# Performance work log

Measured on AMD Instinct MI355X. Metric: run time of the kernel, lower is better.

The kernel has to match this reference:

```python
import jax, jax.numpy as jnp
import numpy as np

B, C, H, W = 4, 2048, 48, 48
HC = 256

def setup_inputs() -> dict:
    key = jax.random.key(0)
    k1, k2, k3, k4 = jax.random.split(key, 4)
    scale = 1.0 / np.sqrt(C)
    return {
        "left_features": jax.random.normal(k1, (B, C, H, W), dtype=jnp.float32),
        "right_features": jax.random.normal(k2, (B, C, H, W), dtype=jnp.float32),
        "Wq": jax.random.normal(k3, (HC, C), dtype=jnp.float32) * scale,
        "bq": jnp.zeros((HC,), dtype=jnp.float32),
        "Wk": jax.random.normal(k4, (HC, C), dtype=jnp.float32) * scale,
        "bk": jnp.zeros((HC,), dtype=jnp.float32),
    }

def _coattn(query_feat, ref_feat, Wq, bq, Wk, bk):
    b, c, h, w = query_feat.shape
    hw = h * w
    # 1x1 convs == per-pixel channel projections
    Q = jnp.einsum('bchw,oc->bohw', query_feat, Wq) + bq[None, :, None, None]
    K = jnp.einsum('bchw,oc->bohw', ref_feat, Wk) + bk[None, :, None, None]
    Qf = Q.reshape(b, -1, hw)          # [b, hc, hw_q]
    Kf = K.reshape(b, -1, hw)          # [b, hc, hw_k]
    V = ref_feat.reshape(b, c, hw)     # [b, c, hw_k]
    # attention scores over all spatial pairs, softmax over reference positions
    attn = jax.nn.softmax(jnp.einsum('bci,bcj->bij', Qf, Kf), axis=-1)  # [b, hw_q, hw_k]
    out = jnp.einsum('bij,bcj->bci', attn, V)  # [b, c, hw_q]
    return out.reshape(b, c, h, w)

def reference(left_features, right_features, Wq, bq, Wk, bk):
    weighted_r = _coattn(left_features, right_features, Wq, bq, Wk, bk)
    weighted_l = _coattn(right_features, left_features, Wq, bq, Wk, bk)
    # rearrange '[orig, weighted] two b c h w -> b (two c) h w' == channel concat
    left_attended = jnp.concatenate([left_features, weighted_l], axis=1)
    right_attended = jnp.concatenate([right_features, weighted_r], axis=1)
    return (left_attended, right_attended)
```

## Files before the change

kernel.cpp:

```cpp
#include <hip/hip_runtime.h>
#include <stdint.h>


#define NB 4
#define NC 2048
#define NHW 2304
#define NHC 256
#define NT 36

typedef _Float16 f16;
typedef __attribute__((ext_vector_type(4))) _Float16 f16x4;
typedef __attribute__((ext_vector_type(8))) _Float16 f16x8;
typedef __attribute__((ext_vector_type(4))) float f32x4;

static __device__ __forceinline__ void glds16(const void* g, void* lds) {
  __builtin_amdgcn_global_load_lds(
      (const __attribute__((address_space(1))) uint32_t*)g,
      (__attribute__((address_space(3))) uint32_t*)lds, 16, 0, 0);
}

__global__ __launch_bounds__(256) void k_prep(
    const float* __restrict__ xl, const float* __restrict__ xr,
    float* __restrict__ out, f16* __restrict__ Xh, f16* __restrict__ Xt) {
  const int z = blockIdx.z, side = z >> 2, b = z & 3;
  const float* X = (side ? xr : xl) + (size_t)b * NC * NHW;
  const int hw0 = blockIdx.x * 64, c0 = blockIdx.y * 64;
  const int t = threadIdx.x;
  const int colb = (t & 15) * 4;
  const int r0 = t >> 4;
  __shared__ f16 Lt[64 * 64];
  float* outb = out + (size_t)side * ((size_t)NB * 2 * NC * NHW) + (size_t)b * (2 * NC * NHW);
  f16* Xhb = Xh + (size_t)side * ((size_t)NB * NC * NHW) + (size_t)b * NC * NHW;
  f16* Xtb = Xt + (size_t)side * ((size_t)NB * NHW * NC) + (size_t)b * NHW * NC;
#pragma unroll
  for (int p = 0; p < 4; ++p) {
    int r = r0 + p * 16;
    size_t go = (size_t)(c0 + r) * NHW + hw0 + colb;
    float4 v = *(const float4*)&X[go];
    *(float4*)&outb[go] = v;
    f16x4 h; h[0] = (f16)v.x; h[1] = (f16)v.y; h[2] = (f16)v.z; h[3] = (f16)v.w;
    *(f16x4*)&Xhb[go] = h;
#pragma unroll
    for (int j = 0; j < 4; ++j) {
      int row = colb + j;
      int byte = row * 128 + ((r * 2) ^ ((((row >> 2) & 7)) << 4));
      *(f16*)((char*)Lt + byte) = h[j];
    }
  }
  __syncthreads();
#pragma unroll
  for (int p = 0; p < 2; ++p) {
    int idx = p * 256 + t;
    int row = idx >> 3, ch = idx & 7;
    int byte = row * 128 + (((ch ^ ((row >> 2) & 7))) << 4);
    f16x8 vv = *(const f16x8*)((char*)Lt + byte);
    *(f16x8*)&Xtb[(size_t)(hw0 + row) * NC + c0 + ch * 8] = vv;
  }
}

__global__ __launch_bounds__(256) void k_w16(
    const float* __restrict__ wq, const float* __restrict__ wk, f16* __restrict__ Ws) {
  const int N4 = NHC * NC / 4;
  int idx = blockIdx.x * 256 + threadIdx.x;
  const float* src = (idx < N4) ? wq : wk;
  int e4 = (idx < N4) ? idx : idx - N4;
  float4 v = ((const float4*)src)[e4];
  f16x4 h; h[0] = (f16)v.x; h[1] = (f16)v.y; h[2] = (f16)v.z; h[3] = (f16)v.w;
  ((f16x4*)Ws)[idx] = h;
}

__global__ __launch_bounds__(256) void k_proj(
    const f16* __restrict__ Ws, const f16* __restrict__ Xt,
    const float* __restrict__ bq, const float* __restrict__ bk,
    f16* __restrict__ Yt) {
  __shared__ f16 LA[2][128 * 32], LB[2][128 * 32];
  const int n0 = blockIdx.x * 128;
  const int m0 = blockIdx.y * 128;
  const int tid = threadIdx.x, wv = tid >> 6, ln = tid & 63;
  const int lr = ln & 15, lh = ln >> 4;
  const int wm = wv >> 1, wn = wv & 1;
  f32x4 acc[4][4];
#pragma unroll
  for (int mi = 0; mi < 4; ++mi)
#pragma unroll
    for (int ni = 0; ni < 4; ++ni)
#pragma unroll
      for (int q = 0; q < 4; ++q) acc[mi][ni][q] = 0.f;

  auto stage = [&](int bi, int ks) {
    int k0 = ks * 32;
#pragma unroll
    for (int rep = 0; rep < 2; ++rep) {
      int u = rep * 256 + wv * 64 + ln;
      int r = u >> 2, k8 = (u & 3) * 8;
      int ub8 = (rep * 256 + wv * 64) * 8;
      glds16(Ws + (size_t)(m0 + r) * NC + k0 + k8, &LA[bi][ub8]);
      glds16(Xt + (size_t)(n0 + r) * NC + k0 + k8, &LB[bi][ub8]);
    }
  };
  auto compute = [&](int bi) {
    f16x8 af[4], bf[4];
#pragma unroll
    for (int mi = 0; mi < 4; ++mi)
      af[mi] = *(const f16x8*)&LA[bi][(wm * 64 + mi * 16 + lr) * 32 + lh * 8];
#pragma unroll
    for (int ni = 0; ni < 4; ++ni)
      bf[ni] = *(const f16x8*)&LB[bi][(wn * 64 + ni * 16 + lr) * 32 + lh * 8];
#pragma unroll
    for (int mi = 0; mi < 4; ++mi)
#pragma unroll
      for (int ni = 0; ni < 4; ++ni)
        acc[mi][ni] = __builtin_amdgcn_mfma_f32_16x16x32_f16(af[mi], bf[ni], acc[mi][ni], 0, 0, 0);
  };

  stage(0, 0);
  __syncthreads();
  int cur = 0;
  for (int ks = 0; ks < 63; ++ks) {
    stage(cur ^ 1, ks + 1);
    compute(cur);
    __syncthreads();
    cur ^= 1;
  }
  compute(cur);

#pragma unroll
  for (int mi = 0; mi < 4; ++mi)
#pragma unroll
    for (int ni = 0; ni < 4; ++ni) {
      int ob = m0 + wm * 64 + mi * 16 + lh * 4;
      int i = n0 + wn * 64 + ni * 16 + lr;
      f16x4 hv;
#pragma unroll
      for (int q = 0; q < 4; ++q) {
        int o = ob + q;
        float bias = (o < NHC) ? bq[o] : bk[o - NHC];
        hv[q] = (f16)(acc[mi][ni][q] + bias);
      }
      *(f16x4*)&Yt[(size_t)i * 512 + ob] = hv;
    }
}

__global__ __launch_bounds__(256) void k_scores(
    const f16* __restrict__ Q, const f16* __restrict__ K, float* __restrict__ S) {
  __shared__ f16 LA[2][128 * 32], LB[2][128 * 32];
  const int b = blockIdx.z;
  const int i0 = blockIdx.x * 128, j0 = blockIdx.y * 128;
  const int tid = threadIdx.x, wv = tid >> 6, ln = tid & 63;
  const int lr = ln & 15, lh = ln >> 4;
  const int wm = wv >> 1, wn = wv & 1;
  const f16* Qb = Q + (size_t)b * NHW * 512;
  const f16* Kb = K + (size_t)b * NHW * 512;
  f32x4 acc[4][4];
#pragma unroll
  for (int mi = 0; mi < 4; ++mi)
#pragma unroll
    for (int ni = 0; ni < 4; ++ni)
#pragma unroll
      for (int q = 0; q < 4; ++q) acc[mi][ni][q] = 0.f;

  auto stage = [&](int bi, int ks) {
    int k0 = ks * 32;
#pragma unroll
    for (int rep = 0; rep < 2; ++rep) {
      int u = rep * 256 + wv * 64 + ln;
      int r = u >> 2, k8 = (u & 3) * 8;
      int ub8 = (rep * 256 + wv * 64) * 8;
      glds16(Qb + (size_t)(i0 + r) * 512 + k0 + k8, &LA[bi][ub8]);
      glds16(Kb + (size_t)(j0 + r) * 512 + k0 + k8, &LB[bi][ub8]);
    }
  };
  auto compute = [&](int bi) {
    f16x8 af[4], bf[4];
#pragma unroll
    for (int mi = 0; mi < 4; ++mi)
      af[mi] = *(const f16x8*)&LA[bi][(wm * 64 + mi * 16 + lr) * 32 + lh * 8];
#pragma unroll
    for (int ni = 0; ni < 4; ++ni)
      bf[ni] = *(const f16x8*)&LB[bi][(wn * 64 + ni * 16 + lr) * 32 + lh * 8];
#pragma unroll
    for (int mi = 0; mi < 4; ++mi)
#pragma unroll
      for (int ni = 0; ni < 4; ++ni)
        acc[mi][ni] = __builtin_amdgcn_mfma_f32_16x16x32_f16(af[mi], bf[ni], acc[mi][ni], 0, 0, 0);
  };

  stage(0, 0);
  __syncthreads();
  int cur = 0;
  for (int ks = 0; ks < 7; ++ks) {
    stage(cur ^ 1, ks + 1);
    compute(cur);
    __syncthreads();
    cur ^= 1;
  }
  compute(cur);

  float* Sb = S + (size_t)b * NHW * NHW;
#pragma unroll
  for (int mi = 0; mi < 4; ++mi)
#pragma unroll
    for (int ni = 0; ni < 4; ++ni) {
      int i = i0 + wm * 64 + mi * 16 + lh * 4;
      int j = j0 + wn * 64 + ni * 16 + lr;
#pragma unroll
      for (int q = 0; q < 4; ++q)
        Sb[(size_t)(i + q) * NHW + j] = acc[mi][ni][q];
    }
}

__global__ __launch_bounds__(256) void k_softmax(
    float* __restrict__ S0, float* __restrict__ S1) {
  const int rid = blockIdx.x;
  const int ROWS = NB * NHW;
  float* rp = (rid < ROWS ? S0 : S1) + (size_t)(rid < ROWS ? rid : rid - ROWS) * NHW;
  const int t = threadIdx.x;
  float v[9];
  float m = -3.4e38f;
#pragma unroll
  for (int k = 0; k < 9; ++k) { v[k] = rp[t + 256 * k]; m = fmaxf(m, v[k]); }
#pragma unroll
  for (int off = 32; off > 0; off >>= 1) m = fmaxf(m, __shfl_xor(m, off));
  __shared__ float red[4];
  __shared__ float red2[4];
  const int wv = t >> 6, ln = t & 63;
  if (ln == 0) red[wv] = m;
  __syncthreads();
  m = fmaxf(fmaxf(red[0], red[1]), fmaxf(red[2], red[3]));
  float s = 0.f;
#pragma unroll
  for (int k = 0; k < 9; ++k) { v[k] = expf(v[k] - m); s += v[k]; }
#pragma unroll
  for (int off = 32; off > 0; off >>= 1) s += __shfl_xor(s, off);
  if (ln == 0) red2[wv] = s;
  __syncthreads();
  float inv = 1.0f / (red2[0] + red2[1] + red2[2] + red2[3]);
  f16* op = (f16*)rp;
#pragma unroll
  for (int k = 0; k < 9; ++k) op[t + 256 * k] = (f16)(v[k] * inv);
}

__global__ __launch_bounds__(512, 2) void k_pv8(
    const f16* __restrict__ V0, const f16* __restrict__ V1,
    const float* __restrict__ S0, const float* __restrict__ S1,
    float* __restrict__ out, int ndirs, long long ob0, long long ob1) {
  extern __shared__ __align__(16) f16 SH[];
  f16* LA = SH;
  f16* LB = SH + 3 * 16384;

  const int nwg = ndirs * 576;
  const int bid = blockIdx.x;
  const int wg = (bid & 7) * (nwg >> 3) + (bid >> 3);
  const int n = wg % 18;
  const int r1 = wg / 18;
  const int m = r1 & 7;
  const int r2 = r1 >> 3;
  const int b = r2 & 3;
  const int dir = r2 >> 2;

  const f16* Vb = (dir ? V1 : V0) + (size_t)b * NC * NHW;
  const char* Sb = (const char*)(dir ? S1 : S0) + (size_t)b * NHW * NHW * 4;
  const long long obase = dir ? ob1 : ob0;
  const int c0 = m * 256, i0 = n * 128;
  const int tid = threadIdx.x, wv = tid >> 6, ln = tid & 63;
  const int lr = ln & 15, lg = ln >> 4;
  const int wm = wv >> 1, wn = wv & 1;

  const int fr = tid >> 3;
  const int scolb = ((tid & 7) * 16) ^ ((fr & 7) << 4);
  const f16* aSrc = Vb + (size_t)(c0 + fr) * NHW + (scolb >> 1);
  const char* bSrc = Sb + (size_t)(i0 + fr) * 9216 + scolb;
  const int ldsW = wv * 512;

  auto stA = [&](int s, int t2, int r) {
    glds16(aSrc + (size_t)r * 64 * NHW + t2 * 64, LA + s * 16384 + r * 4096 + ldsW);
  };
  auto stB = [&](int s, int t2, int r) {
    glds16(bSrc + (size_t)r * 64 * 9216 + t2 * 128, LB + s * 8192 + r * 4096 + ldsW);
  };
  auto rdA = [&](int s, int mi, int ks) -> f16x8 {
    int row = wm * 64 + mi * 16 + lr;
    int colb = (ks * 64 + lg * 16) ^ ((row & 7) << 4);
    return *(const f16x8*)((const char*)(LA + s * 16384) + row * 128 + colb);
  };
  auto rdB = [&](int s, int ni, int ks) -> f16x8 {
    int row = wn * 64 + ni * 16 + lr;
    int colb = (ks * 64 + lg * 16) ^ ((row & 7) << 4);
    return *(const f16x8*)((const char*)(LB + s * 8192) + row * 128 + colb);
  };

  f32x4 acc[4][4];
#pragma unroll
  for (int mi = 0; mi < 4; ++mi)
#pragma unroll
    for (int ni = 0; ni < 4; ++ni)
#pragma unroll
      for (int q = 0; q < 4; ++q) acc[mi][ni][q] = 0.f;

  f16x8 A0[4][2], B0[4][2], A1[4][2], B1[4][2];

#pragma unroll
  for (int r = 0; r < 4; ++r) stA(0, 0, r);
  stB(0, 0, 0); stB(0, 0, 1);
#pragma unroll
  for (int r = 0; r < 4; ++r) stA(1, 1, r);
  stB(1, 1, 0); stB(1, 1, 1);
  asm volatile("s_waitcnt vmcnt(6)" ::: "memory");
  asm volatile("s_barrier" ::: "memory");
#pragma unroll
  for (int mi = 0; mi < 4; ++mi) { A0[mi][0] = rdA(0, mi, 0); A0[mi][1] = rdA(0, mi, 1); }
#pragma unroll
  for (int ni = 0; ni < 4; ++ni) { B0[ni][0] = rdB(0, ni, 0); B0[ni][1] = rdB(0, ni, 1); }

  auto step = [&](int t, int s, f16x8 (&Ac)[4][2], f16x8 (&Bc)[4][2],
                  f16x8 (&Ap)[4][2], f16x8 (&Bp)[4][2]) {
    int s2 = s + 2; if (s2 >= 3) s2 -= 3;
    int s1 = s + 1; if (s1 >= 3) s1 -= 3;
    if (t + 2 < NT) {
      stA(s2, t + 2, 0); stA(s2, t + 2, 1); stA(s2, t + 2, 2); stA(s2, t + 2, 3);
      stB(s2, t + 2, 0); stB(s2, t + 2, 1);
      asm volatile("s_waitcnt vmcnt(6)" ::: "memory");
    } else {
      asm volatile("s_waitcnt vmcnt(0)" ::: "memory");
    }
    asm volatile("s_barrier" ::: "memory");
    if (t + 1 < NT) {
#pragma unroll
      for (int mi = 0; mi < 4; ++mi) { Ap[mi][0] = rdA(s1, mi, 0); Ap[mi][1] = rdA(s1, mi, 1); }
#pragma unroll
      for (int ni = 0; ni < 4; ++ni) { Bp[ni][0] = rdB(s1, ni, 0); Bp[ni][1] = rdB(s1, ni, 1); }
    }
    __builtin_amdgcn_s_setprio(1);
#pragma unroll
    for (int ks = 0; ks < 2; ++ks)
#pragma unroll
      for (int mi = 0; mi < 4; ++mi)
#pragma unroll
        for (int ni = 0; ni < 4; ++ni)
          acc[mi][ni] = __builtin_amdgcn_mfma_f32_16x16x32_f16(Ac[mi][ks], Bc[ni][ks], acc[mi][ni], 0, 0, 0);
    __builtin_amdgcn_s_setprio(0);
    asm volatile("s_barrier" ::: "memory");
  };

  int s = 0;
  for (int t = 0; t < NT; t += 2) {
    step(t, s, A0, B0, A1, B1);
    int sn = s + 1; if (sn >= 3) sn -= 3;
    step(t + 1, sn, A1, B1, A0, B0);
    s = s + 2; if (s >= 3) s -= 3;
  }

  float* ob = out + obase + (size_t)b * (2 * NC * NHW);
#pragma unroll
  for (int mi = 0; mi < 4; ++mi)
#pragma unroll
    for (int ni = 0; ni < 4; ++ni) {
      int c = c0 + wm * 64 + mi * 16 + lg * 4;
      int i = i0 + wn * 64 + ni * 16 + lr;
#pragma unroll
      for (int q = 0; q < 4; ++q)
        ob[(size_t)(NC + c + q) * NHW + i] = acc[mi][ni][q];
    }
}

extern "C" void kernel_launch(void* const* d_in, const int* in_sizes, int n_in,
                              void* d_out, int out_size, void* d_ws, size_t ws_size,
                              hipStream_t stream) {
  const float* xl = (const float*)d_in[0];
  const float* xr = (const float*)d_in[1];
  const float* wq = (const float*)d_in[2];
  const float* bq = (const float*)d_in[3];
  const float* wk = (const float*)d_in[4];
  const float* bk = (const float*)d_in[5];
  float* out = (float*)d_out;
  char* ws = (char*)d_ws;

  const size_t XH_BYTES = (size_t)2 * NB * NC * NHW * 2;
  const size_t WS_BYTES = (size_t)512 * NC * 2;
  const size_t YT_BYTES = (size_t)2 * NB * NHW * 512 * 2;
  const size_t S_BYTES  = (size_t)NB * NHW * NHW * 4;

  f16* Xh = (f16*)ws;
  f16* Ws_ = (f16*)(ws + XH_BYTES);
  f16* Yt = (f16*)(ws + XH_BYTES + WS_BYTES);
  char* rest = ws + XH_BYTES + WS_BYTES + YT_BYTES;

  const size_t xh_side = (size_t)NB * NC * NHW;
  const size_t xt_side = (size_t)NB * NHW * NC;
  const size_t yt_side = (size_t)NB * NHW * 512;
  const long long obA = (long long)NB * 2 * NC * NHW;
  const long long obB = 0;

  const bool merged = ws_size >= XH_BYTES + WS_BYTES + YT_BYTES + 2 * S_BYTES;

  if (merged) {
    float* S0 = (float*)rest;
    char* rest2 = rest + S_BYTES;
    f16* Xt = (f16*)rest2;
    float* S1 = (float*)rest2;

    k_prep<<<dim3(36, 32, 8), dim3(256), 0, stream>>>(xl, xr, out, Xh, Xt);
    k_w16<<<dim3(1024), dim3(256), 0, stream>>>(wq, wk, Ws_);
    k_proj<<<dim3(72, 4), dim3(256), 0, stream>>>(Ws_, Xt, bq, bk, Yt);
    k_proj<<<dim3(72, 4), dim3(256), 0, stream>>>(Ws_, Xt + xt_side, bq, bk, Yt + yt_side);

    k_scores<<<dim3(18, 18, NB), dim3(256), 0, stream>>>(Yt, Yt + yt_side + NHC, S0);
    k_scores<<<dim3(18, 18, NB), dim3(256), 0, stream>>>(Yt + yt_side, Yt + NHC, S1);
    k_softmax<<<dim3(2 * NB * NHW), dim3(256), 0, stream>>>(S0, S1);
    k_pv8<<<dim3(1152), dim3(512), 147456, stream>>>(
        Xh + xh_side, Xh, S0, S1, out, 2, obA, obB);
  } else {
    f16* Xt = (f16*)rest;
    float* S = (float*)rest;

    k_prep<<<dim3(36, 32, 8), dim3(256), 0, stream>>>(xl, xr, out, Xh, Xt);
    k_w16<<<dim3(1024), dim3(256), 0, stream>>>(wq, wk, Ws_);
    k_proj<<<dim3(72, 4), dim3(256), 0, stream>>>(Ws_, Xt, bq, bk, Yt);
    k_proj<<<dim3(72, 4), dim3(256), 0, stream>>>(Ws_, Xt + xt_side, bq, bk, Yt + yt_side);

    k_scores<<<dim3(18, 18, NB), dim3(256), 0, stream>>>(Yt, Yt + yt_side + NHC, S);
    k_softmax<<<dim3(NB * NHW), dim3(256), 0, stream>>>(S, S);
    k_pv8<<<dim3(576), dim3(512), 147456, stream>>>(
        Xh + xh_side, Xh + xh_side, S, S, out, 1, obA, obA);

    k_scores<<<dim3(18, 18, NB), dim3(256), 0, stream>>>(Yt + yt_side, Yt + NHC, S);
    k_softmax<<<dim3(NB * NHW), dim3(256), 0, stream>>>(S, S);
    k_pv8<<<dim3(576), dim3(512), 147456, stream>>>(
        Xh, Xh, S, S, out, 1, obB, obB);
  }
}
```

Measured before the change: 522.9 us.

## Enlarge PV GEMM tile to 256x256 with double-buffered split LDS loads

The PV kernel's output tile grows from 256x128 to 256x256 per workgroup, so each wave now owns 128x64 instead of 64x64. The triple-buffered LDS ring with register prefetch becomes a 2-stage ping-pong buffer, and the next tile's global-to-LDS loads are interleaved between three MFMA sub-phases. The intent is to raise arithmetic intensity and halve redundant reloads of the V and score tiles. In exchange it doubles the accumulators (more VGPRs, possibly lower occupancy), adds extra barriers, and halves the grid to 576 blocks.

```diff
diff --git a/kernel.cpp b/kernel.cpp
--- a/kernel.cpp
+++ b/kernel.cpp
@@ -245,14 +245,12 @@
     const float* __restrict__ S0, const float* __restrict__ S1,
     float* __restrict__ out, int ndirs, long long ob0, long long ob1) {
   extern __shared__ __align__(16) f16 SH[];
-  f16* LA = SH;
-  f16* LB = SH + 3 * 16384;
-
-  const int nwg = ndirs * 576;
+
+  const int nwg = ndirs * 288;
   const int bid = blockIdx.x;
   const int wg = (bid & 7) * (nwg >> 3) + (bid >> 3);
-  const int n = wg % 18;
-  const int r1 = wg / 18;
+  const int n = wg % 9;
+  const int r1 = wg / 9;
   const int m = r1 & 7;
   const int r2 = r1 >> 3;
   const int b = r2 & 3;
@@ -261,10 +259,10 @@
   const f16* Vb = (dir ? V1 : V0) + (size_t)b * NC * NHW;
   const char* Sb = (const char*)(dir ? S1 : S0) + (size_t)b * NHW * NHW * 4;
   const long long obase = dir ? ob1 : ob0;
-  const int c0 = m * 256, i0 = n * 128;
+  const int c0 = m * 256, i0 = n * 256;
   const int tid = threadIdx.x, wv = tid >> 6, ln = tid & 63;
   const int lr = ln & 15, lg = ln >> 4;
-  const int wm = wv >> 1, wn = wv & 1;
+  const int wm = wv >> 2, wn = wv & 3;
 
   const int fr = tid >> 3;
   const int scolb = ((tid & 7) * 16) ^ ((fr & 7) << 4);
@@ -272,90 +270,104 @@
   const char* bSrc = Sb + (size_t)(i0 + fr) * 9216 + scolb;
   const int ldsW = wv * 512;
 
-  auto stA = [&](int s, int t2, int r) {
-    glds16(aSrc + (size_t)r * 64 * NHW + t2 * 64, LA + s * 16384 + r * 4096 + ldsW);
-  };
-  auto stB = [&](int s, int t2, int r) {
-    glds16(bSrc + (size_t)r * 64 * 9216 + t2 * 128, LB + s * 8192 + r * 4096 + ldsW);
-  };
-  auto rdA = [&](int s, int mi, int ks) -> f16x8 {
-    int row = wm * 64 + mi * 16 + lr;
+  auto stA = [&](int bf, int t2, int r) {
+    glds16(aSrc + (size_t)r * 64 * NHW + (size_t)t2 * 64,
+           SH + bf * 32768 + r * 4096 + ldsW);
+  };
+  auto stB = [&](int bf, int t2, int r) {
+    glds16(bSrc + (size_t)r * 64 * 9216 + t2 * 128,
+           SH + bf * 32768 + 16384 + r * 4096 + ldsW);
+  };
+  auto rdA = [&](int bf, int mi, int ks) -> f16x8 {
+    int row = wm * 128 + mi * 16 + lr;
     int colb = (ks * 64 + lg * 16) ^ ((row & 7) << 4);
-    return *(const f16x8*)((const char*)(LA + s * 16384) + row * 128 + colb);
-  };
-  auto rdB = [&](int s, int ni, int ks) -> f16x8 {
+    return *(const f16x8*)((const char*)(SH + bf * 32768) + row * 128 + colb);
+  };
+  auto rdB = [&](int bf, int ni, int ks) -> f16x8 {
     int row = wn * 64 + ni * 16 + lr;
     int colb = (ks * 64 + lg * 16) ^ ((row & 7) << 4);
-    return *(const f16x8*)((const char*)(LB + s * 8192) + row * 128 + colb);
-  };
-
-  f32x4 acc[4][4];
-#pragma unroll
-  for (int mi = 0; mi < 4; ++mi)
+    return *(const f16x8*)((const char*)(SH + bf * 32768 + 16384) + row * 128 + colb);
+  };
+
+  f32x4 acc[8][4];
+#pragma unroll
+  for (int mi = 0; mi < 8; ++mi)
 #pragma unroll
     for (int ni = 0; ni < 4; ++ni)
 #pragma unroll
       for (int q = 0; q < 4; ++q) acc[mi][ni][q] = 0.f;
 
-  f16x8 A0[4][2], B0[4][2], A1[4][2], B1[4][2];
+  f16x8 Af[4][2], Bn0[2][2], Bn1[2][2];
 
 #pragma unroll
   for (int r = 0; r < 4; ++r) stA(0, 0, r);
-  stB(0, 0, 0); stB(0, 0, 1);
-#pragma unroll
-  for (int r = 0; r < 4; ++r) stA(1, 1, r);
-  stB(1, 1, 0); stB(1, 1, 1);
-  asm volatile("s_waitcnt vmcnt(6)" ::: "memory");
+#pragma unroll
+  for (int r = 0; r < 4; ++r) stB(0, 0, r);
+  asm volatile("s_waitcnt vmcnt(0)" ::: "memory");
   asm volatile("s_barrier" ::: "memory");
-#pragma unroll
-  for (int mi = 0; mi < 4; ++mi) { A0[mi][0] = rdA(0, mi, 0); A0[mi][1] = rdA(0, mi, 1); }
-#pragma unroll
-  for (int ni = 0; ni < 4; ++ni) { B0[ni][0] = rdB(0, ni, 0); B0[ni][1] = rdB(0, ni, 1); }
-
-  auto step = [&](int t, int s, f16x8 (&Ac)[4][2], f16x8 (&Bc)[4][2],
-                  f16x8 (&Ap)[4][2], f16x8 (&Bp)[4][2]) {
-    int s2 = s + 2; if (s2 >= 3) s2 -= 3;
-    int s1 = s + 1; if (s1 >= 3) s1 -= 3;
-    if (t + 2 < NT) {
-      stA(s2, t + 2, 0); stA(s2, t + 2, 1); stA(s2, t + 2, 2); stA(s2, t + 2, 3);
-      stB(s2, t + 2, 0); stB(s2, t + 2, 1);
-      asm volatile("s_waitcnt vmcnt(6)" ::: "memory");
-    } else {
-      asm volatile("s_waitcnt vmcnt(0)" ::: "memory");
-    }
-    asm volatile("s_barrier" ::: "memory");
-    if (t + 1 < NT) {
-#pragma unroll
-      for (int mi = 0; mi < 4; ++mi) { Ap[mi][0] = rdA(s1, mi, 0); Ap[mi][1] = rdA(s1, mi, 1); }
-#pragma unroll
-      for (int ni = 0; ni < 4; ++ni) { Bp[ni][0] = rdB(s1, ni, 0); Bp[ni][1] = rdB(s1, ni, 1); }
-    }
+
+  for (int t = 0; t < NT; ++t) {
+    const int cb = t & 1, nb = cb ^ 1;
+    const bool st = (t + 1 < NT);
+#pragma unroll
+    for (int mi = 0; mi < 4; ++mi) { Af[mi][0] = rdA(cb, mi, 0); Af[mi][1] = rdA(cb, mi, 1); }
+#pragma unroll
+    for (int ni = 0; ni < 2; ++ni) { Bn0[ni][0] = rdB(cb, ni, 0); Bn0[ni][1] = rdB(cb, ni, 1); }
+    if (st) { stA(nb, t + 1, 0); stA(nb, t + 1, 1); stB(nb, t + 1, 0); stB(nb, t + 1, 1); }
+    asm volatile("s_barrier" ::: "memory");
     __builtin_amdgcn_s_setprio(1);
 #pragma unroll
     for (int ks = 0; ks < 2; ++ks)
 #pragma unroll
       for (int mi = 0; mi < 4; ++mi)
 #pragma unroll
-        for (int ni = 0; ni < 4; ++ni)
-          acc[mi][ni] = __builtin_amdgcn_mfma_f32_16x16x32_f16(Ac[mi][ks], Bc[ni][ks], acc[mi][ni], 0, 0, 0);
+        for (int ni = 0; ni < 2; ++ni)
+          acc[mi][ni] = __builtin_amdgcn_mfma_f32_16x16x32_f16(Af[mi][ks], Bn0[ni][ks], acc[mi][ni], 0, 0, 0);
     __builtin_amdgcn_s_setprio(0);
     asm volatile("s_barrier" ::: "memory");
-  };
-
-  int s = 0;
-  for (int t = 0; t < NT; t += 2) {
-    step(t, s, A0, B0, A1, B1);
-    int sn = s + 1; if (sn >= 3) sn -= 3;
-    step(t + 1, sn, A1, B1, A0, B0);
-    s = s + 2; if (s >= 3) s -= 3;
+#pragma unroll
+    for (int ni = 0; ni < 2; ++ni) { Bn1[ni][0] = rdB(cb, 2 + ni, 0); Bn1[ni][1] = rdB(cb, 2 + ni, 1); }
+    if (st) { stA(nb, t + 1, 2); stA(nb, t + 1, 3); stB(nb, t + 1, 2); stB(nb, t + 1, 3); }
+    asm volatile("s_barrier" ::: "memory");
+    __builtin_amdgcn_s_setprio(1);
+#pragma unroll
+    for (int ks = 0; ks < 2; ++ks)
+#pragma unroll
+      for (int mi = 0; mi < 4; ++mi)
+#pragma unroll
+        for (int ni = 0; ni < 2; ++ni)
+          acc[mi][2 + ni] = __builtin_amdgcn_mfma_f32_16x16x32_f16(Af[mi][ks], Bn1[ni][ks], acc[mi][2 + ni], 0, 0, 0);
+    __builtin_amdgcn_s_setprio(0);
+    asm volatile("s_barrier" ::: "memory");
+#pragma unroll
+    for (int mi = 0; mi < 4; ++mi) { Af[mi][0] = rdA(cb, 4 + mi, 0); Af[mi][1] = rdA(cb, 4 + mi, 1); }
+    asm volatile("s_barrier" ::: "memory");
+    __builtin_amdgcn_s_setprio(1);
+#pragma unroll
+    for (int ks = 0; ks < 2; ++ks)
+#pragma unroll
+      for (int mi = 0; mi < 4; ++mi)
+#pragma unroll
+        for (int ni = 0; ni < 2; ++ni)
+          acc[4 + mi][2 + ni] = __builtin_amdgcn_mfma_f32_16x16x32_f16(Af[mi][ks], Bn1[ni][ks], acc[4 + mi][2 + ni], 0, 0, 0);
+#pragma unroll
+    for (int ks = 0; ks < 2; ++ks)
+#pragma unroll
+      for (int mi = 0; mi < 4; ++mi)
+#pragma unroll
+        for (int ni = 0; ni < 2; ++ni)
+          acc[4 + mi][ni] = __builtin_amdgcn_mfma_f32_16x16x32_f16(Af[mi][ks], Bn0[ni][ks], acc[4 + mi][ni], 0, 0, 0);
+    __builtin_amdgcn_s_setprio(0);
+    asm volatile("s_waitcnt vmcnt(0)" ::: "memory");
+    asm volatile("s_barrier" ::: "memory");
   }
 
   float* ob = out + obase + (size_t)b * (2 * NC * NHW);
 #pragma unroll
-  for (int mi = 0; mi < 4; ++mi)
+  for (int mi = 0; mi < 8; ++mi)
 #pragma unroll
     for (int ni = 0; ni < 4; ++ni) {
-      int c = c0 + wm * 64 + mi * 16 + lg * 4;
+      int c = c0 + wm * 128 + mi * 16 + lg * 4;
       int i = i0 + wn * 64 + ni * 16 + lr;
 #pragma unroll
       for (int q = 0; q < 4; ++q)
@@ -407,7 +419,7 @@
     k_scores<<<dim3(18, 18, NB), dim3(256), 0, stream>>>(Yt, Yt + yt_side + NHC, S0);
     k_scores<<<dim3(18, 18, NB), dim3(256), 0, stream>>>(Yt + yt_side, Yt + NHC, S1);
     k_softmax<<<dim3(2 * NB * NHW), dim3(256), 0, stream>>>(S0, S1);
-    k_pv8<<<dim3(1152), dim3(512), 147456, stream>>>(
+    k_pv8<<<dim3(576), dim3(512), 131072, stream>>>(
         Xh + xh_side, Xh, S0, S1, out, 2, obA, obB);
   } else {
     f16* Xt = (f16*)rest;
@@ -420,12 +432,12 @@
 
     k_scores<<<dim3(18, 18, NB), dim3(256), 0, stream>>>(Yt, Yt + yt_side + NHC, S);
     k_softmax<<<dim3(NB * NHW), dim3(256), 0, stream>>>(S, S);
-    k_pv8<<<dim3(576), dim3(512), 147456, stream>>>(
+    k_pv8<<<dim3(288), dim3(512), 131072, stream>>>(
         Xh + xh_side, Xh + xh_side, S, S, out, 1, obA, obA);
 
     k_scores<<<dim3(18, 18, NB), dim3(256), 0, stream>>>(Yt + yt_side, Yt + NHC, S);
     k_softmax<<<dim3(NB * NHW), dim3(256), 0, stream>>>(S, S);
-    k_pv8<<<dim3(576), dim3(512), 147456, stream>>>(
+    k_pv8<<<dim3(288), dim3(512), 131072, stream>>>(
         Xh, Xh, S, S, out, 1, obB, obB);
   }
 }
```

New measurement: 508.9 us. 2.7% less time.
